# Optimization experiments

Measured on AMD Instinct MI355X. Metric: run time of the kernel, lower is better.

The kernel has to match this reference:

```python
import jax, jax.numpy as jnp
import numpy as np

HIDDEN = 32
FEATURES = 16
LABELS = 4
T = 8
N = 40000
E = 640000
D_IN = FEATURES + LABELS + HIDDEN + 1  # GATv2Conv input dim = 53


def setup_inputs() -> dict:
    key = jax.random.key(0)
    ks = jax.random.split(key, 16)
    x = jax.random.normal(ks[0], (T, N, FEATURES), dtype=jnp.float32)
    mask = (jax.random.uniform(ks[1], (N,)) < 0.7).astype(jnp.float32)
    labels = jax.random.normal(ks[2], (N, LABELS), dtype=jnp.float32)
    edge_index = jax.random.randint(ks[3], (2, E), 0, N, dtype=jnp.int32)
    edge_weight = jax.random.uniform(ks[4], (E,), dtype=jnp.float32)
    s = 1.0 / np.sqrt(D_IN)
    # 4 GATv2Conv layers stacked: 0=reset, 1=update, 2=cell, 3=final
    Wl = jax.random.normal(ks[5], (4, HIDDEN, D_IN), dtype=jnp.float32) * s
    bl = jnp.zeros((4, HIDDEN), dtype=jnp.float32)
    Wr = jax.random.normal(ks[6], (4, HIDDEN, D_IN), dtype=jnp.float32) * s
    br = jnp.zeros((4, HIDDEN), dtype=jnp.float32)
    att = jax.random.normal(ks[7], (4, HIDDEN), dtype=jnp.float32) * (1.0 / np.sqrt(HIDDEN))
    bconv = jnp.zeros((4, HIDDEN), dtype=jnp.float32)
    W1 = jax.random.normal(ks[8], (FEATURES, HIDDEN), dtype=jnp.float32) * (1.0 / np.sqrt(HIDDEN))
    b1 = jnp.zeros((FEATURES,), dtype=jnp.float32)
    W2 = jax.random.normal(ks[9], (FEATURES, 2 * HIDDEN), dtype=jnp.float32) * (1.0 / np.sqrt(2 * HIDDEN))
    b2 = jnp.zeros((FEATURES,), dtype=jnp.float32)
    return {"x": x, "mask": mask, "labels": labels, "edge_index": edge_index,
            "edge_weight": edge_weight, "Wl": Wl, "bl": bl, "Wr": Wr, "br": br,
            "att": att, "bconv": bconv, "W1": W1, "b1": b1, "W2": W2, "b2": b2}


def gatv2(xin, src, dst, Wl, bl, Wr, br, att, bconv):
    # GATv2Conv, heads=1, add_self_loops=False (edge_weight unused: lin_edge is None)
    xl = xin @ Wl.T + bl          # [N, H] source transform (message)
    xr = xin @ Wr.T + br          # [N, H] target transform
    z = jax.nn.leaky_relu(xl[src] + xr[dst], 0.2)  # [E, H]
    e = z @ att                   # [E] attention logits
    m = jax.ops.segment_max(e, dst, num_segments=N)
    a = jnp.exp(e - m[dst])
    den = jax.ops.segment_sum(a, dst, num_segments=N)[dst]
    a = a / jnp.where(den > 0, den, 1.0)
    out = jax.ops.segment_sum(a[:, None] * xl[src], dst, num_segments=N)
    return out + bconv


def reference(x, mask, labels, edge_index, edge_weight, Wl, bl, Wr, br, att, bconv, W1, b1, W2, b2):
    src, dst = edge_index[0], edge_index[1]
    mcol = mask[:, None]                       # [N, 1] float, concatenated as a feature
    mbool = mcol > 0.5                         # [N, 1] bool, used for where()
    masked_input = jnp.where(mbool[None], x, 0.0)  # [T, N, F]
    hidden0 = jnp.ones((N, HIDDEN), dtype=x.dtype)
    x2_0 = masked_input[0]

    def step(carry, xt):
        hidden, x2 = carry
        ft = jnp.concatenate([x2, mcol, labels], axis=1)        # [N, F+1+L]
        inp = jnp.concatenate([ft, hidden], axis=1)             # [N, D_IN]
        reset = jax.nn.sigmoid(gatv2(inp, src, dst, Wl[0], bl[0], Wr[0], br[0], att[0], bconv[0]))
        update = jax.nn.sigmoid(gatv2(inp, src, dst, Wl[1], bl[1], Wr[1], br[1], att[1], bconv[1]))
        cin = jnp.concatenate([ft, reset * hidden], axis=1)
        cell = jnp.tanh(gatv2(cin, src, dst, Wl[2], bl[2], Wr[2], br[2], att[2], bconv[2]))
        hidden = update * hidden + (1.0 - update) * cell        # (dropout inactive: eval mode)
        y1 = hidden @ W1.T + b1
        x1 = jnp.where(mbool, xt, y1)
        ft2 = jnp.concatenate([x1, mcol, hidden, labels], axis=1)  # [N, D_IN]
        s = jax.nn.relu(gatv2(ft2, src, dst, Wl[3], bl[3], Wr[3], br[3], att[3], bconv[3]))
        y2 = jnp.concatenate([s, hidden], axis=1) @ W2.T + b2
        x2_new = jnp.where(mbool, xt, y2)
        return (hidden, x2_new), x2_new

    _, out = jax.lax.scan(step, (hidden0, x2_0), masked_input)
    return out  # [T, N, F]
```

## Files before the change

kernel.cpp:

```cpp
#include <hip/hip_runtime.h>
#include <math.h>

#define NN   40000
#define EE   640000
#define HID  32
#define FEAT 16
#define LAB  4
#define TT   8
#define DIN  53
#define WD   (HID * DIN)


__device__ __forceinline__ unsigned short f2bf(float f) {
    unsigned int u = __float_as_uint(f);
    unsigned int r = u + 0x7fffu + ((u >> 16) & 1u);
    return (unsigned short)(r >> 16);
}
__device__ __forceinline__ float bflo(unsigned int u) { return __uint_as_float(u << 16); }
__device__ __forceinline__ float bfhi(unsigned int u) { return __uint_as_float(u & 0xffff0000u); }
__device__ __forceinline__ void unpack8(uint4 u, float* v) {
    v[0] = bflo(u.x); v[1] = bfhi(u.x);
    v[2] = bflo(u.y); v[3] = bfhi(u.y);
    v[4] = bflo(u.z); v[5] = bfhi(u.z);
    v[6] = bflo(u.w); v[7] = bfhi(u.w);
}


__global__ __launch_bounds__(256) void zero_i32(int* __restrict__ p, int n) {
    int i = blockIdx.x * 256 + threadIdx.x;
    if (i < n) p[i] = 0;
}

__global__ __launch_bounds__(256) void hist_kernel(const int* __restrict__ dst,
                                                   int* __restrict__ deg) {
    int e = blockIdx.x * 256 + threadIdx.x;
    if (e < EE) atomicAdd(&deg[dst[e]], 1);
}

__global__ __launch_bounds__(1024) void scan_kernel(const int* __restrict__ deg,
                                                    int* __restrict__ row_ptr) {
    __shared__ int wsum[16];
    __shared__ int chunk_total;
    int tid = threadIdx.x;
    int lane = tid & 63, wv = tid >> 6;
    int carry = 0;
    if (tid == 0) row_ptr[0] = 0;
    for (int base = 0; base < NN; base += 1024) {
        int i = base + tid;
        int v = (i < NN) ? deg[i] : 0;
        #pragma unroll
        for (int o = 1; o < 64; o <<= 1) {
            int t = __shfl_up(v, o);
            if (lane >= o) v += t;
        }
        if (lane == 63) wsum[wv] = v;
        __syncthreads();
        if (tid < 16) {
            int s = wsum[tid];
            #pragma unroll
            for (int o = 1; o < 16; o <<= 1) {
                int t = __shfl_up(s, o);
                if (tid >= o) s += t;
            }
            wsum[tid] = s;
            if (tid == 15) chunk_total = s;
        }
        __syncthreads();
        int woff = (wv == 0) ? 0 : wsum[wv - 1];
        if (i < NN) row_ptr[i + 1] = carry + woff + v;
        carry += chunk_total;
        __syncthreads();
    }
}

__global__ __launch_bounds__(256) void scatter_kernel(const int* __restrict__ src,
                                                      const int* __restrict__ dst,
                                                      const int* __restrict__ row_ptr,
                                                      int* __restrict__ cursor,
                                                      int* __restrict__ csr_src) {
    int e = blockIdx.x * 256 + threadIdx.x;
    if (e < EE) {
        int d = dst[e];
        int pos = atomicAdd(&cursor[d], 1);
        csr_src[row_ptr[d] + pos] = src[e];
    }
}

__global__ __launch_bounds__(256) void sort_kernel(const int* __restrict__ row_ptr,
                                                   int* __restrict__ csr_src) {
    int wid = threadIdx.x >> 6, lane = threadIdx.x & 63;
    int n = blockIdx.x * 4 + wid;
    if (n >= NN) return;
    int beg = row_ptr[n], end = row_ptr[n + 1];
    int deg = end - beg;
    if (deg <= 1) return;
    if (deg <= 64) {
        int v = (lane < deg) ? csr_src[beg + lane] : 0x7fffffff;
        #pragma unroll
        for (int k = 2; k <= 64; k <<= 1) {
            #pragma unroll
            for (int jj = k >> 1; jj >= 1; jj >>= 1) {
                int pv = __shfl_xor(v, jj);
                bool up = ((lane & k) == 0);
                bool lower = ((lane & jj) == 0);
                int mn = min(v, pv), mx = max(v, pv);
                v = (lower == up) ? mn : mx;
            }
        }
        if (lane < deg) csr_src[beg + lane] = v;
    } else if (lane == 0) {
        for (int i = beg + 1; i < end; ++i) {
            int key = csr_src[i];
            int j = i - 1;
            while (j >= beg && csr_src[j] > key) {
                csr_src[j + 1] = csr_src[j];
                --j;
            }
            csr_src[j + 1] = key;
        }
    }
}


__global__ __launch_bounds__(256) void init_kernel(const float* __restrict__ x0,
                                                   const float* __restrict__ mask,
                                                   float* __restrict__ hidden,
                                                   float* __restrict__ x2) {
    int i = blockIdx.x * 256 + threadIdx.x;
    if (i < NN * HID) hidden[i] = 1.0f;
    if (i < NN * FEAT) {
        int node = i >> 4;
        x2[i] = (mask[node] > 0.5f) ? x0[i] : 0.0f;
    }
}


__global__ __launch_bounds__(256) void dense01_kernel(const float* __restrict__ feat,
                                                      const float* __restrict__ mask,
                                                      const float* __restrict__ labels,
                                                      const float* __restrict__ hsrc,
                                                      const float* __restrict__ Wl,
                                                      const float* __restrict__ bl,
                                                      const float* __restrict__ Wr,
                                                      const float* __restrict__ br,
                                                      unsigned short* __restrict__ xl01h,
                                                      float* __restrict__ xr01) {
    __shared__ float W_s[4 * WD];
    __shared__ float inp_s[8][DIN];
    for (int idx = threadIdx.x; idx < WD; idx += 256) {
        W_s[idx]          = Wl[idx];
        W_s[WD + idx]     = Wl[WD + idx];
        W_s[2 * WD + idx] = Wr[idx];
        W_s[3 * WD + idx] = Wr[WD + idx];
    }
    int ni = threadIdx.x >> 5, k = threadIdx.x & 31;
    const float* w0 = &W_s[k * DIN];
    const float* w1 = &W_s[WD + k * DIN];
    const float* w2 = &W_s[2 * WD + k * DIN];
    const float* w3 = &W_s[3 * WD + k * DIN];
    float bl0 = bl[k], bl1 = bl[HID + k], br0 = br[k], br1 = br[HID + k];
#pragma unroll
    for (int it = 0; it < 4; ++it) {
        int node = blockIdx.x * 32 + it * 8 + ni;
        __syncthreads();
        for (int i = k; i < DIN; i += 32) {
            float v;
            if (i < 16)       v = feat[node * 16 + i];
            else if (i == 16) v = mask[node];
            else if (i < 21)  v = labels[node * 4 + (i - 17)];
            else              v = hsrc[node * 32 + (i - 21)];
            inp_s[ni][i] = v;
        }
        __syncthreads();
        float l0 = bl0, l1 = bl1, r0 = br0, r1 = br1;
#pragma unroll
        for (int i = 0; i < DIN; ++i) {
            float xv = inp_s[ni][i];
            l0 += xv * w0[i];
            l1 += xv * w1[i];
            r0 += xv * w2[i];
            r1 += xv * w3[i];
        }
        xl01h[node * 64 + k]      = f2bf(l0);
        xl01h[node * 64 + 32 + k] = f2bf(l1);
        xr01[node * 64 + k]      = r0;
        xr01[node * 64 + 32 + k] = r1;
    }
}


__device__ __forceinline__ float edge_score8(const float* v, const float* xr, const float* at) {
    float part = 0.0f;
#pragma unroll
    for (int i = 0; i < 8; ++i) {
        float z = v[i] + xr[i];
        z = (z > 0.0f) ? z : 0.2f * z;
        part += z * at[i];
    }
    part += __shfl_xor(part, 1);
    part += __shfl_xor(part, 2);
    return part;
}

__device__ __forceinline__ void online_update8(float e, float& m, float& den, float* acc,
                                               const float* v) {
    if (e > m) {
        float sc = __expf(m - e);
        den *= sc;
#pragma unroll
        for (int i = 0; i < 8; ++i) acc[i] *= sc;
        m = e;
    }
    float a = __expf(e - m);
    den += a;
#pragma unroll
    for (int i = 0; i < 8; ++i) acc[i] += a * v[i];
}

__device__ __forceinline__ void merge_full(float m, float den, const float* acc,
                                           bool ne, float* o) {
    if (ne) {
        float mt = m;
        mt = fmaxf(mt, __shfl_xor(mt, 4));
        mt = fmaxf(mt, __shfl_xor(mt, 8));
        mt = fmaxf(mt, __shfl_xor(mt, 16));
        mt = fmaxf(mt, __shfl_xor(mt, 32));
        float sc = __expf(m - mt);
        float d = den * sc;
        d += __shfl_xor(d, 4);
        d += __shfl_xor(d, 8);
        d += __shfl_xor(d, 16);
        d += __shfl_xor(d, 32);
#pragma unroll
        for (int i = 0; i < 8; ++i) {
            float t = acc[i] * sc;
            t += __shfl_xor(t, 4);
            t += __shfl_xor(t, 8);
            t += __shfl_xor(t, 16);
            t += __shfl_xor(t, 32);
            o[i] = t / d;
        }
    } else {
#pragma unroll
        for (int i = 0; i < 8; ++i) o[i] = 0.0f;
    }
}

__device__ __forceinline__ void merge_half(float m, float den, const float* acc,
                                           bool ne, float* o) {
    if (ne) {
        float mt = m;
        mt = fmaxf(mt, __shfl_xor(mt, 4));
        mt = fmaxf(mt, __shfl_xor(mt, 8));
        mt = fmaxf(mt, __shfl_xor(mt, 16));
        float sc = __expf(m - mt);
        float d = den * sc;
        d += __shfl_xor(d, 4);
        d += __shfl_xor(d, 8);
        d += __shfl_xor(d, 16);
#pragma unroll
        for (int i = 0; i < 8; ++i) {
            float t = acc[i] * sc;
            t += __shfl_xor(t, 4);
            t += __shfl_xor(t, 8);
            t += __shfl_xor(t, 16);
            o[i] = t / d;
        }
    } else {
#pragma unroll
        for (int i = 0; i < 8; ++i) o[i] = 0.0f;
    }
}


__global__ __launch_bounds__(256) void conv01_d2_kernel(
        const int* __restrict__ row_ptr, const int* __restrict__ csr_src,
        const unsigned short* __restrict__ xl01h, const float* __restrict__ xr01,
        const float* __restrict__ att, const float* __restrict__ bconv,
        const float* __restrict__ x2, const float* __restrict__ mask,
        const float* __restrict__ labels, const float* __restrict__ hidden,
        const float* __restrict__ Wl2, const float* __restrict__ bl2,
        const float* __restrict__ Wr2, const float* __restrict__ br2,
        float* __restrict__ g1,
        unsigned short* __restrict__ xlh, float* __restrict__ xr) {
    __shared__ float Wl_s[WD];
    __shared__ float Wr_s[WD];
    __shared__ float cin_s[4][DIN + 3];
    for (int idx = threadIdx.x; idx < WD; idx += 256) {
        Wl_s[idx] = Wl2[idx];
        Wr_s[idx] = Wr2[idx];
    }
    __syncthreads();

    int wid  = threadIdx.x >> 6;
    int lane = threadIdx.x & 63;
    int h  = lane >> 5;
    int hl = lane & 31;
    int g = hl >> 2, j = hl & 3;
    int n = blockIdx.x * 4 + wid;
    int c0 = j * 8;
    int beg = row_ptr[n], end = row_ptr[n + 1];

    float at[8], xrv[8];
    {
        float4 a0 = *(const float4*)(att + h * 32 + c0);
        float4 a1 = *(const float4*)(att + h * 32 + c0 + 4);
        at[0] = a0.x; at[1] = a0.y; at[2] = a0.z; at[3] = a0.w;
        at[4] = a1.x; at[5] = a1.y; at[6] = a1.z; at[7] = a1.w;
        float4 r0 = *(const float4*)(xr01 + n * 64 + h * 32 + c0);
        float4 r1 = *(const float4*)(xr01 + n * 64 + h * 32 + c0 + 4);
        xrv[0] = r0.x; xrv[1] = r0.y; xrv[2] = r0.z; xrv[3] = r0.w;
        xrv[4] = r1.x; xrv[5] = r1.y; xrv[6] = r1.z; xrv[7] = r1.w;
    }

    float m = -INFINITY, den = 0.0f, acc[8] = {0, 0, 0, 0, 0, 0, 0, 0};
    for (int p = beg + g; p < end; p += 8) {
        int s = csr_src[p];
        uint4 u = *(const uint4*)(xl01h + (size_t)s * 64 + h * 32 + c0);
        float v[8];
        unpack8(u, v);
        float e = edge_score8(v, xrv, at);
        online_update8(e, m, den, acc, v);
    }
    float o[8];
    merge_half(m, den, acc, beg < end, o);

    const float* bc = bconv + h * 32 + c0;
    float r[8];
#pragma unroll
    for (int i = 0; i < 8; ++i) r[i] = 1.0f / (1.0f + __expf(-(o[i] + bc[i])));

    if (h == 1 && g == 0) {
        float* p1 = g1 + n * 32 + c0;
        ((float4*)p1)[0] = make_float4(r[0], r[1], r[2], r[3]);
        ((float4*)p1)[1] = make_float4(r[4], r[5], r[6], r[7]);
    }
    if (h == 0 && g == 0) {
        float4 h0 = *(const float4*)(hidden + n * 32 + c0);
        float4 h1 = *(const float4*)(hidden + n * 32 + c0 + 4);
        float hv[8] = {h0.x, h0.y, h0.z, h0.w, h1.x, h1.y, h1.z, h1.w};
#pragma unroll
        for (int i = 0; i < 8; ++i) cin_s[wid][21 + c0 + i] = r[i] * hv[i];
    }
    if (h == 1 && hl < 21) {
        int i = hl;
        float v;
        if (i < 16)       v = x2[n * 16 + i];
        else if (i == 16) v = mask[n];
        else              v = labels[n * 4 + (i - 17)];
        cin_s[wid][i] = v;
    }
    int k = lane & 31;
    const float* w = (h == 0) ? &Wl_s[k * DIN] : &Wr_s[k * DIN];
    float a2 = (h == 0) ? bl2[k] : br2[k];
#pragma unroll
    for (int i = 0; i < DIN; ++i) a2 += cin_s[wid][i] * w[i];
    if (h == 0) xlh[n * 32 + k] = f2bf(a2);
    else        xr[n * 32 + k]  = a2;
}


__global__ __launch_bounds__(256) void conv2_ud3_kernel(
        const int* __restrict__ row_ptr, const int* __restrict__ csr_src,
        const unsigned short* __restrict__ xlh, const float* __restrict__ xr,
        const float* __restrict__ att2, const float* __restrict__ bconv2,
        const float* __restrict__ g1, float* __restrict__ hidden,
        const float* __restrict__ x_t, const float* __restrict__ mask,
        const float* __restrict__ labels,
        const float* __restrict__ W1, const float* __restrict__ b1,
        const float* __restrict__ Wl3, const float* __restrict__ bl3,
        const float* __restrict__ Wr3, const float* __restrict__ br3,
        unsigned short* __restrict__ xlh2, float* __restrict__ xr2) {
    __shared__ float Wl_s[WD];
    __shared__ float Wr_s[WD];
    __shared__ float W1_s[FEAT * HID];
    __shared__ float ft2_s[4][DIN + 3];
    __shared__ float hs[4][HID + 1];
    for (int idx = threadIdx.x; idx < WD; idx += 256) {
        Wl_s[idx] = Wl3[idx];
        Wr_s[idx] = Wr3[idx];
    }
    for (int idx = threadIdx.x; idx < FEAT * HID; idx += 256) W1_s[idx] = W1[idx];
    __syncthreads();

    int wid  = threadIdx.x >> 6;
    int lane = threadIdx.x & 63;
    int g = lane >> 2, j = lane & 3;
    int n = blockIdx.x * 4 + wid;
    int c0 = j * 8;
    int beg = row_ptr[n], end = row_ptr[n + 1];

    float at[8], xrv[8];
    {
        float4 a0 = *(const float4*)(att2 + c0);
        float4 a1 = *(const float4*)(att2 + c0 + 4);
        at[0] = a0.x; at[1] = a0.y; at[2] = a0.z; at[3] = a0.w;
        at[4] = a1.x; at[5] = a1.y; at[6] = a1.z; at[7] = a1.w;
        float4 r0 = *(const float4*)(xr + n * 32 + c0);
        float4 r1 = *(const float4*)(xr + n * 32 + c0 + 4);
        xrv[0] = r0.x; xrv[1] = r0.y; xrv[2] = r0.z; xrv[3] = r0.w;
        xrv[4] = r1.x; xrv[5] = r1.y; xrv[6] = r1.z; xrv[7] = r1.w;
    }

    float m = -INFINITY, den = 0.0f, acc[8] = {0, 0, 0, 0, 0, 0, 0, 0};
    for (int p = beg + g; p < end; p += 16) {
        int s = csr_src[p];
        uint4 u = *(const uint4*)(xlh + (size_t)s * 32 + c0);
        float v[8];
        unpack8(u, v);
        float e = edge_score8(v, xrv, at);
        online_update8(e, m, den, acc, v);
    }
    float o[8];
    merge_full(m, den, acc, beg < end, o);

    {
        const float* bc = bconv2 + c0;
        float4 h0 = *(const float4*)(hidden + n * 32 + c0);
        float4 h1 = *(const float4*)(hidden + n * 32 + c0 + 4);
        float hvv[8] = {h0.x, h0.y, h0.z, h0.w, h1.x, h1.y, h1.z, h1.w};
        float4 u0 = *(const float4*)(g1 + n * 32 + c0);
        float4 u1 = *(const float4*)(g1 + n * 32 + c0 + 4);
        float uv[8] = {u0.x, u0.y, u0.z, u0.w, u1.x, u1.y, u1.z, u1.w};
        float hn[8];
#pragma unroll
        for (int i = 0; i < 8; ++i) {
            float cell = tanhf(o[i] + bc[i]);
            hn[i] = uv[i] * hvv[i] + (1.0f - uv[i]) * cell;
        }
        if (g == 0) {
            float* hp = hidden + n * 32 + c0;
            ((float4*)hp)[0] = make_float4(hn[0], hn[1], hn[2], hn[3]);
            ((float4*)hp)[1] = make_float4(hn[4], hn[5], hn[6], hn[7]);
#pragma unroll
            for (int i = 0; i < 8; ++i) {
                hs[wid][c0 + i] = hn[i];
                ft2_s[wid][17 + c0 + i] = hn[i];
            }
        }
    }
    if (lane == 4) ft2_s[wid][16] = mask[n];
    if (lane >= 8 && lane < 12) ft2_s[wid][49 + (lane - 8)] = labels[n * 4 + (lane - 8)];
    if (lane >= 48) {
        int f = lane - 48;
        float a = b1[f];
        const float* w1r = &W1_s[f * 32];
#pragma unroll
        for (int c = 0; c < 32; ++c) a += hs[wid][c] * w1r[c];
        ft2_s[wid][f] = (mask[n] > 0.5f) ? x_t[n * 16 + f] : a;
    }
    int k = lane & 31;
    int h2 = lane >> 5;
    const float* w = (h2 == 0) ? &Wl_s[k * DIN] : &Wr_s[k * DIN];
    float a3 = (h2 == 0) ? bl3[k] : br3[k];
#pragma unroll
    for (int i = 0; i < DIN; ++i) a3 += ft2_s[wid][i] * w[i];
    if (h2 == 0) xlh2[n * 32 + k] = f2bf(a3);
    else         xr2[n * 32 + k]  = a3;
}


__global__ __launch_bounds__(256) void conv3_out_kernel(const int* __restrict__ row_ptr,
                                                        const int* __restrict__ csr_src,
                                                        const unsigned short* __restrict__ xlh,
                                                        const float* __restrict__ xr,
                                                        const float* __restrict__ att,
                                                        const float* __restrict__ bconv,
                                                        const float* __restrict__ hidden,
                                                        const float* __restrict__ W2,
                                                        const float* __restrict__ b2,
                                                        const float* __restrict__ x_t,
                                                        const float* __restrict__ mask,
                                                        float* __restrict__ x2,
                                                        float* __restrict__ out_t) {
    __shared__ float W2s[64 * 16];
    for (int idx = threadIdx.x; idx < 64 * 16; idx += 256) {
        int f = idx & 15, c = idx >> 4;
        W2s[c * 16 + f] = W2[f * 64 + c];
    }
    __syncthreads();

    int wid  = threadIdx.x >> 6;
    int lane = threadIdx.x & 63;
    int g = lane >> 2, j = lane & 3;
    int n = blockIdx.x * 4 + wid;
    int c0 = j * 8;
    int beg = row_ptr[n], end = row_ptr[n + 1];

    float at[8], xrv[8];
    {
        float4 a0 = *(const float4*)(att + c0);
        float4 a1 = *(const float4*)(att + c0 + 4);
        at[0] = a0.x; at[1] = a0.y; at[2] = a0.z; at[3] = a0.w;
        at[4] = a1.x; at[5] = a1.y; at[6] = a1.z; at[7] = a1.w;
        float4 r0 = *(const float4*)(xr + n * 32 + c0);
        float4 r1 = *(const float4*)(xr + n * 32 + c0 + 4);
        xrv[0] = r0.x; xrv[1] = r0.y; xrv[2] = r0.z; xrv[3] = r0.w;
        xrv[4] = r1.x; xrv[5] = r1.y; xrv[6] = r1.z; xrv[7] = r1.w;
    }

    float m = -INFINITY, den = 0.0f, acc[8] = {0, 0, 0, 0, 0, 0, 0, 0};
    for (int p = beg + g; p < end; p += 16) {
        int s = csr_src[p];
        uint4 u = *(const uint4*)(xlh + (size_t)s * 32 + c0);
        float v[8];
        unpack8(u, v);
        float e = edge_score8(v, xrv, at);
        online_update8(e, m, den, acc, v);
    }
    float o[8];
    merge_full(m, den, acc, beg < end, o);

    float r[8], hv[8];
    {
        const float* bc = bconv + c0;
#pragma unroll
        for (int i = 0; i < 8; ++i) r[i] = fmaxf(o[i] + bc[i], 0.0f);
        float4 h0 = *(const float4*)(hidden + n * 32 + c0);
        float4 h1 = *(const float4*)(hidden + n * 32 + c0 + 4);
        hv[0] = h0.x; hv[1] = h0.y; hv[2] = h0.z; hv[3] = h0.w;
        hv[4] = h1.x; hv[5] = h1.y; hv[6] = h1.z; hv[7] = h1.w;
    }

    int f = lane & 15;
    int base = lane & ~3;
    float y = b2[f];
#pragma unroll
    for (int j2 = 0; j2 < 4; ++j2) {
#pragma unroll
        for (int i = 0; i < 8; ++i) {
            float sv = __shfl(r[i], base + j2);
            float hh = __shfl(hv[i], base + j2);
            int c = j2 * 8 + i;
            y += sv * W2s[c * 16 + f] + hh * W2s[(32 + c) * 16 + f];
        }
    }
    if (lane < 16) {
        float mv = mask[n];
        float xv = x_t[n * 16 + f];
        float rr = (mv > 0.5f) ? xv : y;
        x2[n * 16 + f] = rr;
        out_t[n * 16 + f] = rr;
    }
}


extern "C" void kernel_launch(void* const* d_in, const int* in_sizes, int n_in,
                              void* d_out, int out_size, void* d_ws, size_t ws_size,
                              hipStream_t stream) {
    const float* x      = (const float*)d_in[0];
    const float* mask   = (const float*)d_in[1];
    const float* labels = (const float*)d_in[2];
    const int*   src    = (const int*)d_in[3];
    const int*   dst    = src + EE;
    const float* Wl    = (const float*)d_in[5];
    const float* bl    = (const float*)d_in[6];
    const float* Wr    = (const float*)d_in[7];
    const float* br    = (const float*)d_in[8];
    const float* att   = (const float*)d_in[9];
    const float* bconv = (const float*)d_in[10];
    const float* W1    = (const float*)d_in[11];
    const float* b1    = (const float*)d_in[12];
    const float* W2    = (const float*)d_in[13];
    const float* b2    = (const float*)d_in[14];
    float* out = (float*)d_out;

    char* ws = (char*)d_ws;
    size_t off = 0;
    auto alloc = [&](size_t bytes) -> void* {
        void* p = ws + off;
        off = (off + bytes + 255) & ~(size_t)255;
        return p;
    };
    int*   row_ptr = (int*)alloc((NN + 1) * sizeof(int));
    int*   deg     = (int*)alloc(NN * sizeof(int));
    int*   csr_src = (int*)alloc(EE * sizeof(int));
    float* hidden  = (float*)alloc(NN * HID * sizeof(float));
    float* x2      = (float*)alloc(NN * FEAT * sizeof(float));
    unsigned short* xl01h = (unsigned short*)alloc(NN * 64 * sizeof(unsigned short));
    float* xr01    = (float*)alloc(NN * 64 * sizeof(float));
    unsigned short* xlh  = (unsigned short*)alloc(NN * 32 * sizeof(unsigned short));
    float* xr      = (float*)alloc(NN * HID * sizeof(float));
    unsigned short* xlh2 = (unsigned short*)alloc(NN * 32 * sizeof(unsigned short));
    float* xr2     = (float*)alloc(NN * HID * sizeof(float));
    float* g1      = (float*)alloc(NN * HID * sizeof(float));

    zero_i32<<<(NN + 255) / 256, 256, 0, stream>>>(deg, NN);
    hist_kernel<<<EE / 256, 256, 0, stream>>>(dst, deg);
    scan_kernel<<<1, 1024, 0, stream>>>(deg, row_ptr);
    zero_i32<<<(NN + 255) / 256, 256, 0, stream>>>(deg, NN);
    scatter_kernel<<<EE / 256, 256, 0, stream>>>(src, dst, row_ptr, deg, csr_src);
    sort_kernel<<<NN / 4, 256, 0, stream>>>(row_ptr, csr_src);
    init_kernel<<<NN * HID / 256, 256, 0, stream>>>(x, mask, hidden, x2);

    const int WDc = WD;
    for (int t = 0; t < TT; ++t) {
        const float* xt = x + (size_t)t * NN * FEAT;
        float* out_t = out + (size_t)t * NN * FEAT;
        dense01_kernel<<<NN / 32, 256, 0, stream>>>(x2, mask, labels, hidden,
            Wl, bl, Wr, br, xl01h, xr01);
        conv01_d2_kernel<<<NN / 4, 256, 0, stream>>>(row_ptr, csr_src, xl01h, xr01,
            att, bconv, x2, mask, labels, hidden,
            Wl + 2 * WDc, bl + 2 * HID, Wr + 2 * WDc, br + 2 * HID,
            g1, xlh, xr);
        conv2_ud3_kernel<<<NN / 4, 256, 0, stream>>>(row_ptr, csr_src, xlh, xr,
            att + 2 * HID, bconv + 2 * HID, g1, hidden, xt, mask, labels,
            W1, b1, Wl + 3 * WDc, bl + 3 * HID, Wr + 3 * WDc, br + 3 * HID,
            xlh2, xr2);
        conv3_out_kernel<<<NN / 4, 256, 0, stream>>>(row_ptr, csr_src, xlh2, xr2,
            att + 3 * HID, bconv + 3 * HID, hidden, W2, b2, xt, mask, x2, out_t);
    }
}
```

Measured before the change: 1.904 ms.

## Fuse next-step reset/update dense transform into conv3 output kernel, pad weights

The per-step dense01 kernel is removed from the loop. Its reset/update input projections for the next timestep are now computed at the tail of the conv3 output kernel from the freshly produced x2 and hidden, with one dense01 launch kept before the loop for step zero. Shared-memory weight rows are padded from 53 to 56 so the dot products can use float4 LDS reads, and W1 is transposed in LDS to avoid bank conflicts. This saves one launch and one global round trip per step, at the cost of more LDS per block (four padded weight matrices plus W2), which may lower occupancy in the conv3 kernel. It also does a useless extra projection on the final step.

```diff
diff --git a/kernel.cpp b/kernel.cpp
--- a/kernel.cpp
+++ b/kernel.cpp
@@ -8,7 +8,9 @@
 #define LAB  4
 #define TT   8
 #define DIN  53
+#define DINP 56
 #define WD   (HID * DIN)
+#define WDP  (HID * DINP)
 
 
 __device__ __forceinline__ unsigned short f2bf(float f) {
@@ -23,6 +25,20 @@
     v[2] = bflo(u.y); v[3] = bfhi(u.y);
     v[4] = bflo(u.z); v[5] = bfhi(u.z);
     v[6] = bflo(u.w); v[7] = bfhi(u.w);
+}
+
+__device__ __forceinline__ float dot56(const float* __restrict__ w,
+                                       const float* __restrict__ c, float a) {
+#pragma unroll
+    for (int t = 0; t < 14; ++t) {
+        float4 wv = *(const float4*)(w + t * 4);
+        float4 cv = *(const float4*)(c + t * 4);
+        a += cv.x * wv.x;
+        a += cv.y * wv.y;
+        a += cv.z * wv.z;
+        a += cv.w * wv.w;
+    }
+    return a;
 }
 
 
@@ -272,6 +288,15 @@
     }
 }
 
+__device__ __forceinline__ void stage_padded(float* __restrict__ dstW,
+                                             const float* __restrict__ srcW,
+                                             int tid) {
+    for (int idx = tid; idx < WDP; idx += 256) {
+        int k = idx / DINP, i = idx - k * DINP;
+        dstW[idx] = (i < DIN) ? srcW[k * DIN + i] : 0.0f;
+    }
+}
+
 
 __global__ __launch_bounds__(256) void conv01_d2_kernel(
         const int* __restrict__ row_ptr, const int* __restrict__ csr_src,
@@ -283,13 +308,11 @@
         const float* __restrict__ Wr2, const float* __restrict__ br2,
         float* __restrict__ g1,
         unsigned short* __restrict__ xlh, float* __restrict__ xr) {
-    __shared__ float Wl_s[WD];
-    __shared__ float Wr_s[WD];
-    __shared__ float cin_s[4][DIN + 3];
-    for (int idx = threadIdx.x; idx < WD; idx += 256) {
-        Wl_s[idx] = Wl2[idx];
-        Wr_s[idx] = Wr2[idx];
-    }
+    __shared__ float Wl_s[WDP];
+    __shared__ float Wr_s[WDP];
+    __shared__ float cin_s[4][DINP];
+    stage_padded(Wl_s, Wl2, threadIdx.x);
+    stage_padded(Wr_s, Wr2, threadIdx.x);
     __syncthreads();
 
     int wid  = threadIdx.x >> 6;
@@ -350,11 +373,12 @@
         else              v = labels[n * 4 + (i - 17)];
         cin_s[wid][i] = v;
     }
+    if (h == 1 && hl == 21) {
+        cin_s[wid][53] = 0.0f; cin_s[wid][54] = 0.0f; cin_s[wid][55] = 0.0f;
+    }
     int k = lane & 31;
-    const float* w = (h == 0) ? &Wl_s[k * DIN] : &Wr_s[k * DIN];
-    float a2 = (h == 0) ? bl2[k] : br2[k];
-#pragma unroll
-    for (int i = 0; i < DIN; ++i) a2 += cin_s[wid][i] * w[i];
+    const float* w = (h == 0) ? &Wl_s[k * DINP] : &Wr_s[k * DINP];
+    float a2 = dot56(w, cin_s[wid], (h == 0) ? bl2[k] : br2[k]);
     if (h == 0) xlh[n * 32 + k] = f2bf(a2);
     else        xr[n * 32 + k]  = a2;
 }
@@ -371,16 +395,17 @@
         const float* __restrict__ Wl3, const float* __restrict__ bl3,
         const float* __restrict__ Wr3, const float* __restrict__ br3,
         unsigned short* __restrict__ xlh2, float* __restrict__ xr2) {
-    __shared__ float Wl_s[WD];
-    __shared__ float Wr_s[WD];
-    __shared__ float W1_s[FEAT * HID];
-    __shared__ float ft2_s[4][DIN + 3];
+    __shared__ float Wl_s[WDP];
+    __shared__ float Wr_s[WDP];
+    __shared__ float W1T_s[HID * FEAT];
+    __shared__ float ft2_s[4][DINP];
     __shared__ float hs[4][HID + 1];
-    for (int idx = threadIdx.x; idx < WD; idx += 256) {
-        Wl_s[idx] = Wl3[idx];
-        Wr_s[idx] = Wr3[idx];
-    }
-    for (int idx = threadIdx.x; idx < FEAT * HID; idx += 256) W1_s[idx] = W1[idx];
+    stage_padded(Wl_s, Wl3, threadIdx.x);
+    stage_padded(Wr_s, Wr3, threadIdx.x);
+    for (int idx = threadIdx.x; idx < FEAT * HID; idx += 256) {
+        int f = idx & 15, c = idx >> 4;
+        W1T_s[c * 16 + f] = W1[f * 32 + c];
+    }
     __syncthreads();
 
     int wid  = threadIdx.x >> 6;
@@ -440,44 +465,47 @@
         }
     }
     if (lane == 4) ft2_s[wid][16] = mask[n];
+    if (lane == 5) { ft2_s[wid][53] = 0.0f; ft2_s[wid][54] = 0.0f; ft2_s[wid][55] = 0.0f; }
     if (lane >= 8 && lane < 12) ft2_s[wid][49 + (lane - 8)] = labels[n * 4 + (lane - 8)];
     if (lane >= 48) {
         int f = lane - 48;
         float a = b1[f];
-        const float* w1r = &W1_s[f * 32];
-#pragma unroll
-        for (int c = 0; c < 32; ++c) a += hs[wid][c] * w1r[c];
+#pragma unroll
+        for (int c = 0; c < 32; ++c) a += hs[wid][c] * W1T_s[c * 16 + f];
         ft2_s[wid][f] = (mask[n] > 0.5f) ? x_t[n * 16 + f] : a;
     }
     int k = lane & 31;
     int h2 = lane >> 5;
-    const float* w = (h2 == 0) ? &Wl_s[k * DIN] : &Wr_s[k * DIN];
-    float a3 = (h2 == 0) ? bl3[k] : br3[k];
-#pragma unroll
-    for (int i = 0; i < DIN; ++i) a3 += ft2_s[wid][i] * w[i];
+    const float* w = (h2 == 0) ? &Wl_s[k * DINP] : &Wr_s[k * DINP];
+    float a3 = dot56(w, ft2_s[wid], (h2 == 0) ? bl3[k] : br3[k]);
     if (h2 == 0) xlh2[n * 32 + k] = f2bf(a3);
     else         xr2[n * 32 + k]  = a3;
 }
 
 
-__global__ __launch_bounds__(256) void conv3_out_kernel(const int* __restrict__ row_ptr,
-                                                        const int* __restrict__ csr_src,
-                                                        const unsigned short* __restrict__ xlh,
-                                                        const float* __restrict__ xr,
-                                                        const float* __restrict__ att,
-                                                        const float* __restrict__ bconv,
-                                                        const float* __restrict__ hidden,
-                                                        const float* __restrict__ W2,
-                                                        const float* __restrict__ b2,
-                                                        const float* __restrict__ x_t,
-                                                        const float* __restrict__ mask,
-                                                        float* __restrict__ x2,
-                                                        float* __restrict__ out_t) {
+__global__ __launch_bounds__(256) void conv3_out_d01_kernel(
+        const int* __restrict__ row_ptr, const int* __restrict__ csr_src,
+        const unsigned short* __restrict__ xlh, const float* __restrict__ xr,
+        const float* __restrict__ att3, const float* __restrict__ bconv3,
+        const float* __restrict__ hidden,
+        const float* __restrict__ W2, const float* __restrict__ b2,
+        const float* __restrict__ x_t, const float* __restrict__ mask,
+        const float* __restrict__ labels,
+        const float* __restrict__ Wl01, const float* __restrict__ bl01,
+        const float* __restrict__ Wr01, const float* __restrict__ br01,
+        float* __restrict__ x2, float* __restrict__ out_t,
+        unsigned short* __restrict__ xl01h, float* __restrict__ xr01) {
     __shared__ float W2s[64 * 16];
+    __shared__ float W01_s[4 * WDP];
+    __shared__ float inp_s[4][DINP];
     for (int idx = threadIdx.x; idx < 64 * 16; idx += 256) {
         int f = idx & 15, c = idx >> 4;
         W2s[c * 16 + f] = W2[f * 64 + c];
     }
+    stage_padded(W01_s,           Wl01,      threadIdx.x);
+    stage_padded(W01_s + WDP,     Wl01 + WD, threadIdx.x);
+    stage_padded(W01_s + 2 * WDP, Wr01,      threadIdx.x);
+    stage_padded(W01_s + 3 * WDP, Wr01 + WD, threadIdx.x);
     __syncthreads();
 
     int wid  = threadIdx.x >> 6;
@@ -489,8 +517,8 @@
 
     float at[8], xrv[8];
     {
-        float4 a0 = *(const float4*)(att + c0);
-        float4 a1 = *(const float4*)(att + c0 + 4);
+        float4 a0 = *(const float4*)(att3 + c0);
+        float4 a1 = *(const float4*)(att3 + c0 + 4);
         at[0] = a0.x; at[1] = a0.y; at[2] = a0.z; at[3] = a0.w;
         at[4] = a1.x; at[5] = a1.y; at[6] = a1.z; at[7] = a1.w;
         float4 r0 = *(const float4*)(xr + n * 32 + c0);
@@ -513,7 +541,7 @@
 
     float r[8], hv[8];
     {
-        const float* bc = bconv + c0;
+        const float* bc = bconv3 + c0;
 #pragma unroll
         for (int i = 0; i < 8; ++i) r[i] = fmaxf(o[i] + bc[i], 0.0f);
         float4 h0 = *(const float4*)(hidden + n * 32 + c0);
@@ -541,6 +569,29 @@
         float rr = (mv > 0.5f) ? xv : y;
         x2[n * 16 + f] = rr;
         out_t[n * 16 + f] = rr;
+        inp_s[wid][f] = rr;
+    }
+    if (lane == 16) inp_s[wid][16] = mask[n];
+    if (lane >= 17 && lane < 21) inp_s[wid][lane] = labels[n * 4 + (lane - 17)];
+    if (lane == 21) { inp_s[wid][53] = 0.0f; inp_s[wid][54] = 0.0f; inp_s[wid][55] = 0.0f; }
+    if (g == 0) {
+#pragma unroll
+        for (int i = 0; i < 8; ++i) inp_s[wid][21 + c0 + i] = hv[i];
+    }
+    int k = lane & 31;
+    int h2 = lane >> 5;
+    const float* wa = &W01_s[(h2 * 2 + 0) * WDP + k * DINP];
+    const float* wb = &W01_s[(h2 * 2 + 1) * WDP + k * DINP];
+    float a0 = (h2 == 0) ? bl01[k] : br01[k];
+    float a1 = (h2 == 0) ? bl01[HID + k] : br01[HID + k];
+    a0 = dot56(wa, inp_s[wid], a0);
+    a1 = dot56(wb, inp_s[wid], a1);
+    if (h2 == 0) {
+        xl01h[n * 64 + k]      = f2bf(a0);
+        xl01h[n * 64 + 32 + k] = f2bf(a1);
+    } else {
+        xr01[n * 64 + k]      = a0;
+        xr01[n * 64 + 32 + k] = a1;
     }
 }
 
@@ -593,21 +644,22 @@
     sort_kernel<<<NN / 4, 256, 0, stream>>>(row_ptr, csr_src);
     init_kernel<<<NN * HID / 256, 256, 0, stream>>>(x, mask, hidden, x2);
 
-    const int WDc = WD;
+    dense01_kernel<<<NN / 32, 256, 0, stream>>>(x2, mask, labels, hidden,
+        Wl, bl, Wr, br, xl01h, xr01);
+
     for (int t = 0; t < TT; ++t) {
         const float* xt = x + (size_t)t * NN * FEAT;
         float* out_t = out + (size_t)t * NN * FEAT;
-        dense01_kernel<<<NN / 32, 256, 0, stream>>>(x2, mask, labels, hidden,
-            Wl, bl, Wr, br, xl01h, xr01);
         conv01_d2_kernel<<<NN / 4, 256, 0, stream>>>(row_ptr, csr_src, xl01h, xr01,
             att, bconv, x2, mask, labels, hidden,
-            Wl + 2 * WDc, bl + 2 * HID, Wr + 2 * WDc, br + 2 * HID,
+            Wl + 2 * WD, bl + 2 * HID, Wr + 2 * WD, br + 2 * HID,
             g1, xlh, xr);
         conv2_ud3_kernel<<<NN / 4, 256, 0, stream>>>(row_ptr, csr_src, xlh, xr,
             att + 2 * HID, bconv + 2 * HID, g1, hidden, xt, mask, labels,
-            W1, b1, Wl + 3 * WDc, bl + 3 * HID, Wr + 3 * WDc, br + 3 * HID,
+            W1, b1, Wl + 3 * WD, bl + 3 * HID, Wr + 3 * WD, br + 3 * HID,
             xlh2, xr2);
-        conv3_out_kernel<<<NN / 4, 256, 0, stream>>>(row_ptr, csr_src, xlh2, xr2,
-            att + 3 * HID, bconv + 3 * HID, hidden, W2, b2, xt, mask, x2, out_t);
-    }
-}
+        conv3_out_d01_kernel<<<NN / 4, 256, 0, stream>>>(row_ptr, csr_src, xlh2, xr2,
+            att + 3 * HID, bconv + 3 * HID, hidden, W2, b2, xt, mask, labels,
+            Wl, bl, Wr, br, x2, out_t, xl01h, xr01);
+    }
+}
```

After: 2.661 ms. +39.7%, slower.
